# Kernel tuning notes

Measured on AMD Instinct MI355X. Metric: run time of the kernel, lower is better.

## Reference

```python
import jax, jax.numpy as jnp
import numpy as np

R_GAS = 8314.46261815324   # Cantera gas constant, J/(kmol K)
ONE_ATM = 101325.0
B, S, NR = 2048, 100, 800
POLY = 5


def setup_inputs() -> dict:
    key = jax.random.key(0)
    ks = jax.random.split(key, 11)
    T = jax.random.uniform(ks[0], (B, 1), minval=300.0, maxval=2500.0)
    P = ONE_ATM * jax.random.uniform(ks[1], (B, 1), minval=0.5, maxval=2.0)
    Y = jax.random.uniform(ks[2], (B, S), minval=0.01, maxval=1.0)
    TPY = jnp.concatenate([T, P, Y], axis=1)
    molecular_weights = jax.random.uniform(ks[3], (S, 1), minval=2.0, maxval=100.0)
    # NASA-7 coefficients with realistic per-column magnitudes
    scales = jnp.array([1.0, 1e-3, 1e-6, 1e-9, 1e-12, 1e3, 1.0])
    base = jnp.array([3.5, 0.0, 0.0, 0.0, 0.0, 0.0, 5.0])
    nasa_low = jax.random.normal(ks[4], (S, 7)) * scales + base
    nasa_high = jax.random.normal(ks[5], (S, 7)) * scales + base
    efficiencies_coeffs = jax.random.uniform(ks[6], (S, NR), minval=0.0, maxval=2.0)
    is_three_body = (jax.random.uniform(ks[7], (NR,)) < 0.3).astype(jnp.float32)
    # positive poly coefficients so viscosity/conductivity/diffusion stay > 0
    species_viscosities_poly = jax.random.uniform(ks[8], (POLY, S), minval=1e-6, maxval=1e-5)
    thermal_conductivity_poly = jax.random.uniform(ks[9], (POLY, S), minval=1e-4, maxval=1e-3)
    binary_diff_coeffs_poly = jax.random.uniform(ks[10], (POLY, S * S), minval=1e-7, maxval=1e-6)
    return {
        'TPY': TPY,
        'molecular_weights': molecular_weights,
        'nasa_low': nasa_low,
        'nasa_high': nasa_high,
        'efficiencies_coeffs': efficiencies_coeffs,
        'is_three_body': is_three_body,
        'species_viscosities_poly': species_viscosities_poly,
        'thermal_conductivity_poly': thermal_conductivity_poly,
        'binary_diff_coeffs_poly': binary_diff_coeffs_poly,
    }


def _forward(TPY, mw, nasa_low, nasa_high, eff, i3b, visc_poly, cond_poly, bdiff_poly):
    n_sp = mw.shape[0]
    # ---- set_states: state variables ----
    T = jnp.clip(TPY[:, 0:1], 200.0, None)            # [B,1]
    logT = jnp.log(T)
    P = TPY[:, 1:2]
    Y = jnp.clip(TPY[:, 2:], 0.0, None)
    Y = Y / Y.sum(axis=1, keepdims=True)
    mean_W = 1.0 / (Y @ (1.0 / mw))                   # [B,1]
    rho = P / R_GAS / T * mean_W                      # mass density
    X = Y * mean_W / mw.T                             # mole fractions
    C = Y * rho / mw.T                                # molar concentrations
    mask = (T <= 1000.0).astype(T.dtype)              # [B,1] NASA branch select
    # ---- cp (NASA poly) ----
    cp_T = jnp.concatenate([T**0, T, T**2, T**3, T**4], axis=1)
    cp = (cp_T @ nasa_low[:, :5].T) * mask + (cp_T @ nasa_high[:, :5].T) * (1.0 - mask)
    cp_mole = (R_GAS * cp * X).sum(axis=1)
    # ---- enthalpy ----
    H_T = jnp.concatenate([T**0, T / 2, T**2 / 3, T**3 / 4, T**4 / 5, 1.0 / T], axis=1)
    H = ((H_T @ nasa_low[:, :6].T) * mask + (H_T @ nasa_high[:, :6].T) * (1.0 - mask)) * R_GAS * T
    h = H / mw.T
    enthalpy_mass = (h * Y).sum(axis=1)
    # ---- entropy ----
    idx = jnp.array([0, 1, 2, 3, 4, 6])
    S_T = jnp.concatenate([logT, T, T**2 / 2, T**3 / 3, T**4 / 4, T**0], axis=1)
    S0 = ((S_T @ nasa_low[:, idx].T) * mask + (S_T @ nasa_high[:, idx].T) * (1.0 - mask)) * R_GAS
    S_sp = S0 - R_GAS * jnp.log(X) - R_GAS * jnp.log(P / ONE_ATM)
    s = S_sp / mw.T
    entropy_mass = (s * Y).sum(axis=1)
    # ---- third-body effective concentrations ----
    C_M = C @ eff                                     # [B,NR]
    C_M2 = C_M * i3b + (1.0 - i3b)
    # ---- update_transport: viscosity (Wilke mixing) ----
    poly_order = visc_poly.shape[0]
    trans_T = jnp.concatenate([logT**i for i in range(poly_order - 1, -1, -1)], axis=1)
    sp_visc = trans_T @ visc_poly                     # [B,S]
    Wk_over_Wj = mw @ (1.0 / mw.T)                    # [S,S]
    Wj_over_Wk = 1.0 / Wk_over_Wj
    eta_ratio = sp_visc[:, :, None] / sp_visc[:, None, :]  # [B,S,S]
    PHI = (1.0 / 2.8284271247461903) / jnp.sqrt(1.0 + Wk_over_Wj) \
          * (1.0 + jnp.sqrt(eta_ratio) * Wj_over_Wk**0.25) ** 2
    denom = jnp.einsum('bij,bj->bi', PHI, X)
    viscosities = (X * sp_visc / denom).sum(axis=1, keepdims=True)
    # ---- thermal conductivity ----
    sp_cond = trans_T @ cond_poly
    thermal_conductivity = 0.5 * ((X * sp_cond).sum(axis=1, keepdims=True)
                                  + 1.0 / (X / sp_cond).sum(axis=1, keepdims=True))
    # ---- mixture-averaged diffusion coefficients ----
    bdc = (trans_T @ bdiff_poly).reshape(-1, n_sp, n_sp)    # [B,S,S]
    X_eps = jnp.clip(X, 1e-12, None)
    XjWj = X_eps @ mw - X_eps * mw.T                        # [B,S]
    XjDjk = jnp.einsum('bj,bjk->bk', X_eps, 1.0 / bdc) \
            - X_eps / jnp.diagonal(bdc, axis1=-2, axis2=-1)
    mix_diff = XjWj / XjDjk / mean_W / P * ONE_ATM
    return jnp.concatenate([cp_mole[:, None], enthalpy_mass[:, None], entropy_mass[:, None],
                            C_M2, viscosities, thermal_conductivity, mix_diff], axis=1)


def reference(TPY, molecular_weights, nasa_low, nasa_high, efficiencies_coeffs,
              is_three_body, species_viscosities_poly, thermal_conductivity_poly,
              binary_diff_coeffs_poly):
    return _forward(TPY, molecular_weights, nasa_low, nasa_high, efficiencies_coeffs,
                    is_three_body, species_viscosities_poly, thermal_conductivity_poly,
                    binary_diff_coeffs_poly)
```

## Files before the change

### kernel.cpp

```cpp
#include <hip/hip_runtime.h>
#include <math.h>

namespace {

constexpr int S = 100;
constexpr int NR = 800;
constexpr int RPB = 4;
constexpr int NTH = 1024;
constexpr int IN_COLS = 2 + S;
constexpr int OUT_COLS = 3 + NR + 2 + S;
constexpr float RGASF = 8314.46261815324f;
constexpr float ATMF = 101325.0f;

__device__ __forceinline__ float wave_sum(float v) {
#pragma unroll
  for (int off = 32; off; off >>= 1) v += __shfl_xor(v, off);
  return v;
}

__global__ __launch_bounds__(NTH, 8)
void chem_props_kernel(const float* __restrict__ TPY,
                       const float* __restrict__ mw,
                       const float* __restrict__ nasa_low,
                       const float* __restrict__ nasa_high,
                       const float* __restrict__ eff,
                       const float* __restrict__ i3b,
                       const float* __restrict__ visc_poly,
                       const float* __restrict__ cond_poly,
                       const float* __restrict__ bdiff_poly,
                       float* __restrict__ out)
{
  __shared__ __align__(16) float Xl[S][RPB];
  __shared__ __align__(16) float u1l[S][RPB];
  __shared__ __align__(16) float u2l[S][RPB];
  __shared__ __align__(16) float viscl[S][RPB];
  __shared__ __align__(16) float svl[S][RPB];
  __shared__ __align__(16) float denoml[S][RPB];
  __shared__ __align__(16) float xjdl[S][RPB];
  __shared__ float mwl[S], imwl[S];
  __shared__ float pa[8][2];
  __shared__ float pb[8][5];
  __shared__ float rs_L[RPB], rs_cfac[RPB], rs_mW[RPB], rs_scale[RPB], rs_T[RPB];
  __shared__ float vsum[RPB];

  const int tid = threadIdx.x;
  const int wid = tid >> 6;
  const int lane = tid & 63;
  const int row0 = blockIdx.x * RPB;

  if (tid < S * RPB) {
    (&denoml[0][0])[tid] = 0.0f;
    (&xjdl[0][0])[tid] = 0.0f;
  }
  if (tid < RPB) vsum[tid] = 0.0f;
  if (tid < S) {
    float m = mw[tid];
    mwl[tid] = m;
    imwl[tid] = 1.0f / m;
  }
  __syncthreads();

  float T = 0.f, P = 0.f, L = 0.f, y = 0.f, im = 0.f;
  int row = 0, half = 0, s = 0;
  bool valid = false;
  const float* rowp = nullptr;
  if (wid < 8) {
    row = wid & 3;
    half = wid >> 2;
    rowp = TPY + (size_t)(row0 + row) * IN_COLS;
    T = fmaxf(rowp[0], 200.0f);
    P = rowp[1];
    L = __logf(T);
    s = half * 64 + lane;
    valid = (s < S);
    y = valid ? fmaxf(rowp[2 + s], 0.0f) : 0.0f;
    im = valid ? imwl[s] : 0.0f;
    float py = wave_sum(y);
    float pw = wave_sum(y * im);
    if (lane == 0) { pa[wid][0] = py; pa[wid][1] = pw; }
  }
  __syncthreads();

  if (wid < 8) {
    float T2 = T * T, T3 = T2 * T, T4 = T2 * T2;
    float invT = 1.0f / T;
    float ysum = pa[row][0] + pa[row + 4][0];
    float wsum = pa[row][1] + pa[row + 4][1];
    float invy = 1.0f / ysum;
    float mW = ysum / wsum;
    float cfac = P / (RGASF * T);
    float lnP = __logf(P * (1.0f / ATMF));

    const float* nasa = (T <= 1000.0f) ? nasa_low : nasa_high;

    float cpx = 0.0f, hy = 0.0f, sy = 0.0f, condA = 0.0f, condB = 0.0f;
    if (valid) {
      float yn = y * invy;
      float x = fmaxf(yn * mW * im, 1e-12f);
      const float* a = nasa + s * 7;
      float a0 = a[0], a1 = a[1], a2 = a[2], a3 = a[3],
            a4 = a[4], a5 = a[5], a6 = a[6];
      float cp = a0 + a1 * T + a2 * T2 + a3 * T3 + a4 * T4;
      float Ht = a0 + 0.5f * a1 * T + (1.0f / 3.0f) * a2 * T2
               + 0.25f * a3 * T3 + 0.2f * a4 * T4 + a5 * invT;
      float S0r = a0 * L + a1 * T + 0.5f * a2 * T2
                + (1.0f / 3.0f) * a3 * T3 + 0.25f * a4 * T4 + a6;
      cpx = cp * x;
      hy = Ht * im * yn;
      sy = (S0r - __logf(x) - lnP) * im * yn;

      float v = visc_poly[0 * S + s];
      v = fmaf(v, L, visc_poly[1 * S + s]);
      v = fmaf(v, L, visc_poly[2 * S + s]);
      v = fmaf(v, L, visc_poly[3 * S + s]);
      v = fmaf(v, L, visc_poly[4 * S + s]);
      float c = cond_poly[0 * S + s];
      c = fmaf(c, L, cond_poly[1 * S + s]);
      c = fmaf(c, L, cond_poly[2 * S + s]);
      c = fmaf(c, L, cond_poly[3 * S + s]);
      c = fmaf(c, L, cond_poly[4 * S + s]);
      condA = x * c;
      condB = x / c;
      float sv = sqrtf(v);
      Xl[s][row] = x;
      viscl[s][row] = v;
      svl[s][row] = sv;
      u1l[s][row] = x / sv;
      u2l[s][row] = x / v;
    }
    float scp = wave_sum(cpx);
    float sh = wave_sum(hy);
    float ss = wave_sum(sy);
    float sca = wave_sum(condA);
    float scb = wave_sum(condB);
    if (lane == 0) {
      pb[wid][0] = scp; pb[wid][1] = sh; pb[wid][2] = ss;
      pb[wid][3] = sca; pb[wid][4] = scb;
      if (half == 0) {
        rs_L[row] = L;
        rs_T[row] = T;
        rs_cfac[row] = cfac;
        rs_mW[row] = mW;
        rs_scale[row] = ATMF / (mW * P);
      }
    }
  }
  __syncthreads();

  if (tid < RPB) {
    const int r = tid;
    float scp = pb[r][0] + pb[r + 4][0];
    float sh  = pb[r][1] + pb[r + 4][1];
    float ss  = pb[r][2] + pb[r + 4][2];
    float sca = pb[r][3] + pb[r + 4][3];
    float scb = pb[r][4] + pb[r + 4][4];
    float* orow = out + (size_t)(row0 + r) * OUT_COLS;
    orow[0] = RGASF * scp;
    orow[1] = RGASF * rs_T[r] * sh;
    orow[2] = RGASF * ss;
    orow[3 + NR + 1] = 0.5f * (sca + 1.0f / scb);
  }

  if (tid < NR) {
    const int q = tid;
    float acc[RPB];
#pragma unroll
    for (int b = 0; b < RPB; ++b) acc[b] = 0.0f;
#pragma unroll 4
    for (int s2 = 0; s2 < S; ++s2) {
      float e = eff[s2 * NR + q];
      float xv[RPB];
      *(float4*)&xv[0] = *(const float4*)&Xl[s2][0];
#pragma unroll
      for (int b = 0; b < RPB; ++b) acc[b] = fmaf(xv[b], e, acc[b]);
    }
    float t3 = i3b[q];
    float base = 1.0f - t3;
#pragma unroll
    for (int b = 0; b < RPB; ++b) {
      out[(size_t)(row0 + b) * OUT_COLS + 3 + q] = fmaf(acc[b] * rs_cfac[b], t3, base);
    }
  }

  if (tid < 1000) {
    const int i = tid % 100;
    const int kg = tid / 100;
    const float mwi = mwl[i];
    const float imwi = imwl[i];
    float d0[RPB], d1[RPB], d2[RPB];
#pragma unroll
    for (int b = 0; b < RPB; ++b) { d0[b] = 0; d1[b] = 0; d2[b] = 0; }
    const int k0 = kg * 10;
#pragma unroll 2
    for (int k = k0; k < k0 + 10; ++k) {
      float mwk = mwl[k];
      float A = 0.35355339059327373f *
                __builtin_amdgcn_rsqf(1.0f + mwi * imwl[k]);
      float B4 = sqrtf(sqrtf(mwk * imwi));
      float m1 = A * B4, m2 = m1 * B4;
      float xv[RPB], u1v[RPB], u2v[RPB];
      *(float4*)&xv[0] = *(const float4*)&Xl[k][0];
      *(float4*)&u1v[0] = *(const float4*)&u1l[k][0];
      *(float4*)&u2v[0] = *(const float4*)&u2l[k][0];
#pragma unroll
      for (int b = 0; b < RPB; ++b) {
        d0[b] = fmaf(A, xv[b], d0[b]);
        d1[b] = fmaf(m1, u1v[b], d1[b]);
        d2[b] = fmaf(m2, u2v[b], d2[b]);
      }
    }
#pragma unroll
    for (int b = 0; b < RPB; ++b) {
      float pden = d0[b] + 2.0f * svl[i][b] * d1[b] + viscl[i][b] * d2[b];
      atomicAdd(&denoml[i][b], pden);
    }
  }
  __syncthreads();

  if (tid < 100 * RPB) {
    const int i = tid % 100;
    const int b = tid / 100;
    float contrib = Xl[i][b] * viscl[i][b] / denoml[i][b];
    atomicAdd(&vsum[b], contrib);
  }
  if (tid < 1000) {
    const int k = tid % 100;
    const int jg = tid / 100;
    float Lb[RPB];
#pragma unroll
    for (int b = 0; b < RPB; ++b) Lb[b] = rs_L[b];
    float acc[RPB];
#pragma unroll
    for (int b = 0; b < RPB; ++b) acc[b] = 0.0f;
    const int j0 = jg * 10;
#pragma unroll 2
    for (int j = j0; j < j0 + 10; ++j) {
      if (j == k) continue;
      float c0 = bdiff_poly[0 * 10000 + j * 100 + k];
      float c1 = bdiff_poly[1 * 10000 + j * 100 + k];
      float c2 = bdiff_poly[2 * 10000 + j * 100 + k];
      float c3 = bdiff_poly[3 * 10000 + j * 100 + k];
      float c4 = bdiff_poly[4 * 10000 + j * 100 + k];
      float xv[RPB];
      *(float4*)&xv[0] = *(const float4*)&Xl[j][0];
#pragma unroll
      for (int b = 0; b < RPB; ++b) {
        float p = fmaf(c0, Lb[b], c1);
        p = fmaf(p, Lb[b], c2);
        p = fmaf(p, Lb[b], c3);
        p = fmaf(p, Lb[b], c4);
        acc[b] = fmaf(xv[b], __builtin_amdgcn_rcpf(p), acc[b]);
      }
    }
#pragma unroll
    for (int b = 0; b < RPB; ++b) atomicAdd(&xjdl[k][b], acc[b]);
  }
  __syncthreads();

  if (tid < RPB) {
    out[(size_t)(row0 + tid) * OUT_COLS + 3 + NR] = vsum[tid];
  }
  if (tid < 100 * RPB) {
    const int k = tid % 100;
    const int b = tid / 100;
    float num = rs_mW[b] - Xl[k][b] * mwl[k];
    float md = num / xjdl[k][b] * rs_scale[b];
    out[(size_t)(row0 + b) * OUT_COLS + 3 + NR + 2 + k] = md;
  }
}

}

extern "C" void kernel_launch(void* const* d_in, const int* in_sizes, int n_in,
                              void* d_out, int out_size, void* d_ws, size_t ws_size,
                              hipStream_t stream) {
  const float* TPY        = (const float*)d_in[0];
  const float* mwp        = (const float*)d_in[1];
  const float* nasa_low   = (const float*)d_in[2];
  const float* nasa_high  = (const float*)d_in[3];
  const float* eff        = (const float*)d_in[4];
  const float* i3b        = (const float*)d_in[5];
  const float* visc_poly  = (const float*)d_in[6];
  const float* cond_poly  = (const float*)d_in[7];
  const float* bdiff_poly = (const float*)d_in[8];
  float* out = (float*)d_out;

  const int B = 2048;
  dim3 grid(B / RPB);
  chem_props_kernel<<<grid, NTH, 0, stream>>>(
      TPY, mwp, nasa_low, nasa_high, eff, i3b,
      visc_poly, cond_poly, bdiff_poly, out);
}
```

Baseline: 112.5 us.

## Halve block size and specialize waves for efficiency, viscosity, and diffusion stages

Shrinks the block from 1024 to 512 threads. Work is split by wave roles: 200 threads each compute four reactions with float4 loads of the efficiency matrix, 128 threads compute the full viscosity denominator per species, and 128 threads compute the full diffusion sum per species. This removes the shared-memory atomics, the zero-initialisation and one block barrier. Some transcendentals are replaced with cheaper intrinsics (exp2 of log differences instead of a double sqrt, rsq/rcp), which may cost a little precision. The tradeoff is less parallelism per stage, so each thread runs a longer serial loop.

```diff
diff --git a/kernel.cpp b/kernel.cpp
--- a/kernel.cpp
+++ b/kernel.cpp
@@ -6,7 +6,7 @@
 constexpr int S = 100;
 constexpr int NR = 800;
 constexpr int RPB = 4;
-constexpr int NTH = 1024;
+constexpr int NTH = 512;
 constexpr int IN_COLS = 2 + S;
 constexpr int OUT_COLS = 3 + NR + 2 + S;
 constexpr float RGASF = 8314.46261815324f;
@@ -18,7 +18,11 @@
   return v;
 }
 
-__global__ __launch_bounds__(NTH, 8)
+__device__ __forceinline__ float elem(const float4& v, int i) {
+  return ((const float*)&v)[i];
+}
+
+__global__ __launch_bounds__(NTH, 4)
 void chem_props_kernel(const float* __restrict__ TPY,
                        const float* __restrict__ mw,
                        const float* __restrict__ nasa_low,
@@ -30,58 +34,46 @@
                        const float* __restrict__ bdiff_poly,
                        float* __restrict__ out)
 {
-  __shared__ __align__(16) float Xl[S][RPB];
-  __shared__ __align__(16) float u1l[S][RPB];
-  __shared__ __align__(16) float u2l[S][RPB];
-  __shared__ __align__(16) float viscl[S][RPB];
-  __shared__ __align__(16) float svl[S][RPB];
-  __shared__ __align__(16) float denoml[S][RPB];
-  __shared__ __align__(16) float xjdl[S][RPB];
-  __shared__ float mwl[S], imwl[S];
+  __shared__ __align__(16) float4 XL[S];
+  __shared__ __align__(16) float4 U1[S];
+  __shared__ __align__(16) float4 U2[S];
+  __shared__ __align__(16) float4 VL[S];
+  __shared__ float mwl[S];
+  __shared__ float2 ilm[S];
   __shared__ float pa[8][2];
   __shared__ float pb[8][5];
   __shared__ float rs_L[RPB], rs_cfac[RPB], rs_mW[RPB], rs_scale[RPB], rs_T[RPB];
-  __shared__ float vsum[RPB];
+  __shared__ float psum[2][RPB];
 
   const int tid = threadIdx.x;
   const int wid = tid >> 6;
   const int lane = tid & 63;
   const int row0 = blockIdx.x * RPB;
 
-  if (tid < S * RPB) {
-    (&denoml[0][0])[tid] = 0.0f;
-    (&xjdl[0][0])[tid] = 0.0f;
-  }
-  if (tid < RPB) vsum[tid] = 0.0f;
   if (tid < S) {
     float m = mw[tid];
     mwl[tid] = m;
-    imwl[tid] = 1.0f / m;
-  }
-  __syncthreads();
-
-  float T = 0.f, P = 0.f, L = 0.f, y = 0.f, im = 0.f;
-  int row = 0, half = 0, s = 0;
-  bool valid = false;
-  const float* rowp = nullptr;
-  if (wid < 8) {
-    row = wid & 3;
-    half = wid >> 2;
-    rowp = TPY + (size_t)(row0 + row) * IN_COLS;
-    T = fmaxf(rowp[0], 200.0f);
-    P = rowp[1];
-    L = __logf(T);
-    s = half * 64 + lane;
-    valid = (s < S);
-    y = valid ? fmaxf(rowp[2 + s], 0.0f) : 0.0f;
-    im = valid ? imwl[s] : 0.0f;
+    ilm[tid] = make_float2(1.0f / m, __log2f(m));
+  }
+  __syncthreads();
+
+  const int row = wid & 3;
+  const int half = wid >> 2;
+  const float* rowp = TPY + (size_t)(row0 + row) * IN_COLS;
+  float T = fmaxf(rowp[0], 200.0f);
+  float P = rowp[1];
+  float L = __logf(T);
+  const int s = half * 64 + lane;
+  const bool valid = (s < S);
+  float y = valid ? fmaxf(rowp[2 + s], 0.0f) : 0.0f;
+  float im = valid ? ilm[s].x : 0.0f;
+  {
     float py = wave_sum(y);
     float pw = wave_sum(y * im);
     if (lane == 0) { pa[wid][0] = py; pa[wid][1] = pw; }
   }
   __syncthreads();
-
-  if (wid < 8) {
+  {
     float T2 = T * T, T3 = T2 * T, T4 = T2 * T2;
     float invT = 1.0f / T;
     float ysum = pa[row][0] + pa[row + 4][0];
@@ -90,7 +82,6 @@
     float mW = ysum / wsum;
     float cfac = P / (RGASF * T);
     float lnP = __logf(P * (1.0f / ATMF));
-
     const float* nasa = (T <= 1000.0f) ? nasa_low : nasa_high;
 
     float cpx = 0.0f, hy = 0.0f, sy = 0.0f, condA = 0.0f, condB = 0.0f;
@@ -121,12 +112,10 @@
       c = fmaf(c, L, cond_poly[4 * S + s]);
       condA = x * c;
       condB = x / c;
-      float sv = sqrtf(v);
-      Xl[s][row] = x;
-      viscl[s][row] = v;
-      svl[s][row] = sv;
-      u1l[s][row] = x / sv;
-      u2l[s][row] = x / v;
+      ((float*)&XL[s])[row] = x;
+      ((float*)&VL[s])[row] = v;
+      ((float*)&U1[s])[row] = x * __builtin_amdgcn_rsqf(v);
+      ((float*)&U2[s])[row] = x * __builtin_amdgcn_rcpf(v);
     }
     float scp = wave_sum(cpx);
     float sh = wave_sum(hy);
@@ -161,111 +150,118 @@
     orow[3 + NR + 1] = 0.5f * (sca + 1.0f / scb);
   }
 
-  if (tid < NR) {
-    const int q = tid;
-    float acc[RPB];
-#pragma unroll
-    for (int b = 0; b < RPB; ++b) acc[b] = 0.0f;
+  if (tid < 200) {
+    const int q0 = tid * 4;
+    float acc[4][4];
+#pragma unroll
+    for (int qi = 0; qi < 4; ++qi)
+#pragma unroll
+      for (int b = 0; b < RPB; ++b) acc[qi][b] = 0.0f;
 #pragma unroll 4
     for (int s2 = 0; s2 < S; ++s2) {
-      float e = eff[s2 * NR + q];
-      float xv[RPB];
-      *(float4*)&xv[0] = *(const float4*)&Xl[s2][0];
-#pragma unroll
-      for (int b = 0; b < RPB; ++b) acc[b] = fmaf(xv[b], e, acc[b]);
-    }
-    float t3 = i3b[q];
-    float base = 1.0f - t3;
-#pragma unroll
-    for (int b = 0; b < RPB; ++b) {
-      out[(size_t)(row0 + b) * OUT_COLS + 3 + q] = fmaf(acc[b] * rs_cfac[b], t3, base);
-    }
-  }
-
-  if (tid < 1000) {
-    const int i = tid % 100;
-    const int kg = tid / 100;
-    const float mwi = mwl[i];
-    const float imwi = imwl[i];
-    float d0[RPB], d1[RPB], d2[RPB];
-#pragma unroll
-    for (int b = 0; b < RPB; ++b) { d0[b] = 0; d1[b] = 0; d2[b] = 0; }
-    const int k0 = kg * 10;
+      float4 e = *(const float4*)&eff[s2 * NR + q0];
+      float4 xq = XL[s2];
+#pragma unroll
+      for (int qi = 0; qi < 4; ++qi)
+#pragma unroll
+        for (int b = 0; b < RPB; ++b)
+          acc[qi][b] = fmaf(elem(xq, b), elem(e, qi), acc[qi][b]);
+    }
+    float cf[RPB];
+#pragma unroll
+    for (int b = 0; b < RPB; ++b) cf[b] = rs_cfac[b];
+    float4 t3 = *(const float4*)&i3b[q0];
+#pragma unroll
+    for (int qi = 0; qi < 4; ++qi) {
+      float tq = elem(t3, qi);
+      float base = 1.0f - tq;
+#pragma unroll
+      for (int b = 0; b < RPB; ++b)
+        out[(size_t)(row0 + b) * OUT_COLS + 3 + q0 + qi] =
+            fmaf(acc[qi][b] * cf[b], tq, base);
+    }
+  } else if (tid >= 256 && tid < 384) {
+    const int i = tid - 256;
+    float contrib[RPB] = {0.0f, 0.0f, 0.0f, 0.0f};
+    if (i < S) {
+      const float mwi = mwl[i];
+      const float lmi = ilm[i].y;
+      float d0[RPB], d1[RPB], d2[RPB];
+#pragma unroll
+      for (int b = 0; b < RPB; ++b) { d0[b] = 0; d1[b] = 0; d2[b] = 0; }
 #pragma unroll 2
-    for (int k = k0; k < k0 + 10; ++k) {
+      for (int k = 0; k < S; ++k) {
+        float2 il = ilm[k];
+        float A = 0.35355339059327373f *
+                  __builtin_amdgcn_rsqf(1.0f + mwi * il.x);
+        float B4 = __builtin_amdgcn_exp2f(0.25f * (il.y - lmi));
+        float m1 = A * B4, m2 = m1 * B4;
+        float4 xq = XL[k];
+        float4 u1q = U1[k];
+        float4 u2q = U2[k];
+#pragma unroll
+        for (int b = 0; b < RPB; ++b) {
+          d0[b] = fmaf(A, elem(xq, b), d0[b]);
+          d1[b] = fmaf(m1, elem(u1q, b), d1[b]);
+          d2[b] = fmaf(m2, elem(u2q, b), d2[b]);
+        }
+      }
+      float4 vq = VL[i];
+      float4 xiq = XL[i];
+#pragma unroll
+      for (int b = 0; b < RPB; ++b) {
+        float vi = elem(vq, b);
+        float den = d0[b] + 2.0f * sqrtf(vi) * d1[b] + vi * d2[b];
+        contrib[b] = elem(xiq, b) * vi / den;
+      }
+    }
+#pragma unroll
+    for (int b = 0; b < RPB; ++b) contrib[b] = wave_sum(contrib[b]);
+    if (lane == 0) {
+#pragma unroll
+      for (int b = 0; b < RPB; ++b) psum[wid - 4][b] = contrib[b];
+    }
+  } else if (tid >= 384) {
+    const int k = tid - 384;
+    if (k < S) {
+      float Lb[RPB], acc[RPB];
+#pragma unroll
+      for (int b = 0; b < RPB; ++b) { Lb[b] = rs_L[b]; acc[b] = 0.0f; }
+      const float* bp = bdiff_poly + k;
+#pragma unroll 2
+      for (int j = 0; j < S; ++j) {
+        float c0 = bp[j * 100];
+        float c1 = bp[10000 + j * 100];
+        float c2 = bp[20000 + j * 100];
+        float c3 = bp[30000 + j * 100];
+        float c4 = bp[40000 + j * 100];
+        float4 xq = XL[j];
+        bool diag = (j == k);
+#pragma unroll
+        for (int b = 0; b < RPB; ++b) {
+          float p = fmaf(c0, Lb[b], c1);
+          p = fmaf(p, Lb[b], c2);
+          p = fmaf(p, Lb[b], c3);
+          p = fmaf(p, Lb[b], c4);
+          float r = diag ? 0.0f : __builtin_amdgcn_rcpf(p);
+          acc[b] = fmaf(elem(xq, b), r, acc[b]);
+        }
+      }
+      float4 xkq = XL[k];
       float mwk = mwl[k];
-      float A = 0.35355339059327373f *
-                __builtin_amdgcn_rsqf(1.0f + mwi * imwl[k]);
-      float B4 = sqrtf(sqrtf(mwk * imwi));
-      float m1 = A * B4, m2 = m1 * B4;
-      float xv[RPB], u1v[RPB], u2v[RPB];
-      *(float4*)&xv[0] = *(const float4*)&Xl[k][0];
-      *(float4*)&u1v[0] = *(const float4*)&u1l[k][0];
-      *(float4*)&u2v[0] = *(const float4*)&u2l[k][0];
 #pragma unroll
       for (int b = 0; b < RPB; ++b) {
-        d0[b] = fmaf(A, xv[b], d0[b]);
-        d1[b] = fmaf(m1, u1v[b], d1[b]);
-        d2[b] = fmaf(m2, u2v[b], d2[b]);
-      }
-    }
-#pragma unroll
-    for (int b = 0; b < RPB; ++b) {
-      float pden = d0[b] + 2.0f * svl[i][b] * d1[b] + viscl[i][b] * d2[b];
-      atomicAdd(&denoml[i][b], pden);
-    }
-  }
-  __syncthreads();
-
-  if (tid < 100 * RPB) {
-    const int i = tid % 100;
-    const int b = tid / 100;
-    float contrib = Xl[i][b] * viscl[i][b] / denoml[i][b];
-    atomicAdd(&vsum[b], contrib);
-  }
-  if (tid < 1000) {
-    const int k = tid % 100;
-    const int jg = tid / 100;
-    float Lb[RPB];
-#pragma unroll
-    for (int b = 0; b < RPB; ++b) Lb[b] = rs_L[b];
-    float acc[RPB];
-#pragma unroll
-    for (int b = 0; b < RPB; ++b) acc[b] = 0.0f;
-    const int j0 = jg * 10;
-#pragma unroll 2
-    for (int j = j0; j < j0 + 10; ++j) {
-      if (j == k) continue;
-      float c0 = bdiff_poly[0 * 10000 + j * 100 + k];
-      float c1 = bdiff_poly[1 * 10000 + j * 100 + k];
-      float c2 = bdiff_poly[2 * 10000 + j * 100 + k];
-      float c3 = bdiff_poly[3 * 10000 + j * 100 + k];
-      float c4 = bdiff_poly[4 * 10000 + j * 100 + k];
-      float xv[RPB];
-      *(float4*)&xv[0] = *(const float4*)&Xl[j][0];
-#pragma unroll
-      for (int b = 0; b < RPB; ++b) {
-        float p = fmaf(c0, Lb[b], c1);
-        p = fmaf(p, Lb[b], c2);
-        p = fmaf(p, Lb[b], c3);
-        p = fmaf(p, Lb[b], c4);
-        acc[b] = fmaf(xv[b], __builtin_amdgcn_rcpf(p), acc[b]);
-      }
-    }
-#pragma unroll
-    for (int b = 0; b < RPB; ++b) atomicAdd(&xjdl[k][b], acc[b]);
+        float num = rs_mW[b] - elem(xkq, b) * mwk;
+        out[(size_t)(row0 + b) * OUT_COLS + 3 + NR + 2 + k] =
+            num * __builtin_amdgcn_rcpf(acc[b]) * rs_scale[b];
+      }
+    }
   }
   __syncthreads();
 
   if (tid < RPB) {
-    out[(size_t)(row0 + tid) * OUT_COLS + 3 + NR] = vsum[tid];
-  }
-  if (tid < 100 * RPB) {
-    const int k = tid % 100;
-    const int b = tid / 100;
-    float num = rs_mW[b] - Xl[k][b] * mwl[k];
-    float md = num / xjdl[k][b] * rs_scale[b];
-    out[(size_t)(row0 + b) * OUT_COLS + 3 + NR + 2 + k] = md;
+    out[(size_t)(row0 + tid) * OUT_COLS + 3 + NR] =
+        psum[0][tid] + psum[1][tid];
   }
 }
 
```

Measured after the change: 100.0 us. 11.1% less time.
